# Performance work log

Measured on AMD Instinct MI355X. Metric: run time of the kernel, lower is better.

Reference implementation:

```python
import jax, jax.numpy as jnp
import numpy as np

B, H, W, C = 4, 128, 128, 768
NUM_BLOCKS = 8
BLOCK = C // NUM_BLOCKS  # 96
HSF = 1
SCALE = 0.02
LAMBD = 0.01
HARD_FRAC = 1.0


def setup_inputs() -> dict:
    key = jax.random.key(0)
    ks = jax.random.split(key, 5)
    return {
        "x": jax.random.normal(ks[0], (B, H, W, C), dtype=jnp.float32),
        "w1": SCALE * jax.random.normal(ks[1], (2, NUM_BLOCKS, BLOCK, BLOCK * HSF), dtype=jnp.float32),
        "b1": SCALE * jax.random.normal(ks[2], (2, NUM_BLOCKS, BLOCK * HSF), dtype=jnp.float32),
        "w2": SCALE * jax.random.normal(ks[3], (2, NUM_BLOCKS, BLOCK * HSF, BLOCK), dtype=jnp.float32),
        "b2": SCALE * jax.random.normal(ks[4], (2, NUM_BLOCKS, BLOCK), dtype=jnp.float32),
    }


def softshrink(v, lambd):
    return jnp.where(v > lambd, v - lambd, jnp.where(v < -lambd, v + lambd, 0.0))


def reference(x, w1, b1, w2, b2):
    bias = x
    dtype = x.dtype
    xf = jnp.fft.rfft2(x.astype(jnp.float32), axes=(1, 2), norm="ortho")  # [B,H,Wf,C] complex
    b, h, wf, c = xf.shape
    xf = xf.reshape(b, h, wf, NUM_BLOCKS, BLOCK)
    total_modes = H * W // 2 + 1
    kept = min(int(total_modes * HARD_FRAC), wf)  # static; with frac=1 kept == wf

    xr = jnp.real(xf[:, :, :kept])
    xi = jnp.imag(xf[:, :, :kept])

    o1r = jax.nn.relu(jnp.einsum("bhwni,nio->bhwno", xr, w1[0]) - jnp.einsum("bhwni,nio->bhwno", xi, w1[1]) + b1[0])
    o1i = jax.nn.relu(jnp.einsum("bhwni,nio->bhwno", xi, w1[0]) + jnp.einsum("bhwni,nio->bhwno", xr, w1[1]) + b1[1])

    o2r = jnp.einsum("bhwno,noi->bhwni", o1r, w2[0]) - jnp.einsum("bhwno,noi->bhwni", o1i, w2[1]) + b2[0]
    o2i = jnp.einsum("bhwno,noi->bhwni", o1i, w2[0]) + jnp.einsum("bhwno,noi->bhwni", o1r, w2[1]) + b2[1]

    o2r = softshrink(o2r, LAMBD)
    o2i = softshrink(o2i, LAMBD)

    if kept < wf:  # zero-fill the masked-out high frequencies
        pad = [(0, 0), (0, 0), (0, wf - kept), (0, 0), (0, 0)]
        o2r = jnp.pad(o2r, pad)
        o2i = jnp.pad(o2i, pad)

    xc = (o2r + 1j * o2i).reshape(b, h, wf, c)
    out = jnp.fft.irfft2(xc, s=(H, W), axes=(1, 2), norm="ortho").astype(dtype)
    return out + bias
```

## Files before the change

kernel.cpp:

```cpp
#include <hip/hip_runtime.h>

#define CH    768
#define BC    96
#define HHH   128
#define WWW   128
#define WF    65
#define LAMBD_ 0.01f
#define NPOS  33280
#define SOFF  204472320ull

typedef __bf16 bf16x8 __attribute__((ext_vector_type(8)));
typedef float  f32x4  __attribute__((ext_vector_type(4)));
typedef unsigned short ushort_t;

union U8 { ushort_t u[8]; bf16x8 v; uint4 q; };

__device__ __forceinline__ ushort_t rnbf(float f) {
  unsigned u = __builtin_bit_cast(unsigned, f);
  return (ushort_t)((u + 0x7FFFu + ((u >> 16) & 1u)) >> 16);
}

struct Tab {
  float c[64]; float s[64];
  static constexpr double tsin(double x) {
    double t = x, r = x; const double x2 = x * x;
    for (int i = 1; i <= 15; ++i) { t *= -x2 / ((2.0 * i) * (2.0 * i + 1.0)); r += t; }
    return r;
  }
  static constexpr double tcos(double x) {
    double t = 1.0, r = 1.0; const double x2 = x * x;
    for (int i = 1; i <= 15; ++i) { t *= -x2 / ((2.0 * i - 1.0) * (2.0 * i)); r += t; }
    return r;
  }
  constexpr Tab() : c{}, s{} {
    for (int k = 0; k < 64; ++k) {
      const double a = 6.283185307179586476925287 * (double)k / 128.0;
      c[k] = (float)tcos(a); s[k] = (float)tsin(a);
    }
  }
};
__device__ const Tab DTAB{};

__host__ __device__ constexpr int rev6(int n) {
  int r = 0;
  for (int b = 0; b < 6; ++b) r |= ((n >> b) & 1) << (5 - b);
  return r;
}

template<bool INV>
__device__ __forceinline__ void fft64_reg(float (&zr)[64], float (&zi)[64]) {
#pragma unroll
  for (int s = 1; s <= 6; ++s) {
    const int half = 1 << (s - 1);
#pragma unroll
    for (int i = 0; i < 64; i += (1 << s)) {
#pragma unroll
      for (int j = 0; j < half; ++j) {
        const int tw = j << (7 - s);
        const float wr = DTAB.c[tw];
        const float wi = INV ? DTAB.s[tw] : -DTAB.s[tw];
        const int i0 = i + j, i1 = i0 + half;
        const float xr = zr[i1], xi = zi[i1];
        const float vr = xr * wr - xi * wi;
        const float vi = xr * wi + xi * wr;
        const float ur = zr[i0], ui = zi[i0];
        zr[i0] = ur + vr; zi[i0] = ui + vi;
        zr[i1] = ur - vr; zi[i1] = ui - vi;
      }
    }
  }
}

__global__ __launch_bounds__(256, 1) void k_rfft_w(const float* __restrict__ x,
                                                   float2* __restrict__ S) {
  const int idx = blockIdx.x * 256 + threadIdx.x;
  const int c  = idx % CH;
  const int bh = idx / CH;
  const float* px = x + (size_t)bh * (WWW * CH) + c;
  float zr[64], zi[64];
#pragma unroll
  for (int n = 0; n < 64; ++n) {
    zr[rev6(n)] = px[(size_t)(2 * n) * CH];
    zi[rev6(n)] = px[(size_t)(2 * n + 1) * CH];
  }
  fft64_reg<false>(zr, zi);
  float2* pS = S + (size_t)bh * (WF * CH) + c;
  const float sc = 1.0f / 128.0f;
#pragma unroll
  for (int k = 0; k <= 32; ++k) {
    const int m = (64 - k) & 63;
    const float ar = zr[k], ai = zi[k];
    const float br = zr[m], bi = zi[m];
    const float Er = 0.5f * (ar + br), Ei = 0.5f * (ai - bi);
    const float Or = 0.5f * (ai + bi), Oi = 0.5f * (br - ar);
    const float wr = DTAB.c[k], wi = -DTAB.s[k];
    const float Tr = Or * wr - Oi * wi;
    const float Ti = Or * wi + Oi * wr;
    pS[(size_t)k * CH] = make_float2(sc * (Er + Tr), sc * (Ei + Ti));
    if (k != 32)
      pS[(size_t)(64 - k) * CH] = make_float2(sc * (Er - Tr), sc * (Ti - Ei));
  }
}

template<bool INV>
__global__ __launch_bounds__(256) void k_fft_h(float2* __restrict__ S) {
  __shared__ float lr[128 * 33];
  __shared__ float li[128 * 33];
  const int tid = threadIdx.x;
  const int c = tid & 31;
  const int g = tid >> 5;
  const int ct = blockIdx.x % 24;
  const int t2 = blockIdx.x / 24;
  const int wf = t2 % WF;
  const int b  = t2 / WF;
  float2* base = S + ((size_t)(b * HHH) * WF + wf) * CH + ct * 32 + c;
  const size_t hs = (size_t)WF * CH;
#pragma unroll
  for (int t = 0; t < 16; ++t) {
    const int h = t * 8 + g;
    const float2 v = base[(size_t)h * hs];
    const int hb = (int)(__brev((unsigned)h) >> 25);
    lr[hb * 33 + c] = v.x;
    li[hb * 33 + c] = v.y;
  }
  __syncthreads();
#pragma unroll
  for (int s = 1; s <= 7; ++s) {
    const int half = 1 << (s - 1);
#pragma unroll
    for (int t = 0; t < 8; ++t) {
      const int bf = g * 8 + t;
      const int j  = bf & (half - 1);
      const int i0 = ((bf >> (s - 1)) << s) + j;
      const int i1 = i0 + half;
      const int tw = j << (7 - s);
      const float wr = DTAB.c[tw];
      const float wi = INV ? DTAB.s[tw] : -DTAB.s[tw];
      const float ur = lr[i0 * 33 + c], ui = li[i0 * 33 + c];
      const float xr = lr[i1 * 33 + c], xi = li[i1 * 33 + c];
      const float vr = xr * wr - xi * wi;
      const float vi = xr * wi + xi * wr;
      lr[i0 * 33 + c] = ur + vr;  li[i0 * 33 + c] = ui + vi;
      lr[i1 * 33 + c] = ur - vr;  li[i1 * 33 + c] = ui - vi;
    }
    __syncthreads();
  }
#pragma unroll
  for (int t = 0; t < 16; ++t) {
    const int h = t * 8 + g;
    base[(size_t)h * hs] = make_float2(lr[h * 33 + c], li[h * 33 + c]);
  }
}

__global__ __launch_bounds__(256) void k_pack(const float* __restrict__ w1,
                                              const float* __restrict__ w2,
                                              ushort_t* __restrict__ Bpk) {
  const int t = blockIdx.x * 256 + threadIdx.x;
  const int nl   = t / 36864;
  const int rem  = t % 36864;
  const int ki   = rem / 6144;
  const int rem2 = rem % 6144;
  const int ni   = rem2 / 512;
  const int rem3 = rem2 % 512;
  const int lane = rem3 >> 3, j = rem3 & 7;
  const int n = nl >> 1, layer = nl & 1;
  const int k   = ki * 32 + (lane >> 4) * 8 + j;
  const int col = ni * 16 + (lane & 15);
  const int kk = (k < 96) ? k : k - 96;
  const int cc = (col < 96) ? col : col - 96;
  const int f  = ((k < 96) != (col < 96)) ? 1 : 0;
  const float sgn = (k >= 96 && col < 96) ? -1.f : 1.f;
  const float* w = layer ? w2 : w1;
  const float val = sgn * w[((size_t)(f * 8 + n) * 96 + kk) * 96 + cc];
  Bpk[t] = rnbf(val);
}

__global__ __launch_bounds__(256) void k_mlp2(float2* __restrict__ S,
                                              const ushort_t* __restrict__ Bpk,
                                              const float* __restrict__ b1,
                                              const float* __restrict__ b2) {
  __shared__ ushort_t o1[64 * 200];
  const int tid = threadIdx.x;
  const int l = tid & 63, wid = tid >> 6;
  const int lr = l & 15, lg = l >> 4;
  const int n  = blockIdx.x & 7;
  const int p0 = (blockIdx.x >> 3) * 64 + wid * 16;

  U8 aR[3], aI[3];
  const float4* xbase = (const float4*)(S + (size_t)(p0 + lr) * CH + n * BC);
#pragma unroll
  for (int kp = 0; kp < 3; ++kp) {
    const float4* q = xbase + (kp * 32 + lg * 8) / 2;
    const float4 f0 = q[0], f1 = q[1], f2 = q[2], f3 = q[3];
    aR[kp].u[0] = rnbf(f0.x); aR[kp].u[1] = rnbf(f0.z);
    aR[kp].u[2] = rnbf(f1.x); aR[kp].u[3] = rnbf(f1.z);
    aR[kp].u[4] = rnbf(f2.x); aR[kp].u[5] = rnbf(f2.z);
    aR[kp].u[6] = rnbf(f3.x); aR[kp].u[7] = rnbf(f3.z);
    aI[kp].u[0] = rnbf(f0.y); aI[kp].u[1] = rnbf(f0.w);
    aI[kp].u[2] = rnbf(f1.y); aI[kp].u[3] = rnbf(f1.w);
    aI[kp].u[4] = rnbf(f2.y); aI[kp].u[5] = rnbf(f2.w);
    aI[kp].u[6] = rnbf(f3.y); aI[kp].u[7] = rnbf(f3.w);
  }

  f32x4 acc[12];
#pragma unroll
  for (int ni = 0; ni < 12; ++ni) {
    const int col = ni * 16 + lr;
    const float bv = (col < 96) ? b1[n * 96 + col] : b1[768 + n * 96 + col - 96];
    acc[ni] = (f32x4){bv, bv, bv, bv};
  }
  const uint4* bq1 = (const uint4*)(Bpk + (size_t)(n * 2 + 0) * 36864) + l;
#pragma unroll
  for (int ni = 0; ni < 12; ++ni)
#pragma unroll
    for (int ki = 0; ki < 6; ++ki) {
      U8 b; b.q = bq1[(ki * 12 + ni) * 64];
      const bf16x8 a = (ki < 3) ? aR[ki].v : aI[ki - 3].v;
      acc[ni] = __builtin_amdgcn_mfma_f32_16x16x32_bf16(a, b.v, acc[ni], 0, 0, 0);
    }
#pragma unroll
  for (int ni = 0; ni < 12; ++ni) {
    const int col = ni * 16 + lr;
#pragma unroll
    for (int r = 0; r < 4; ++r) {
      const int grow = wid * 16 + lg * 4 + r;
      o1[grow * 200 + col] = rnbf(fmaxf(acc[ni][r], 0.f));
    }
  }
  __syncthreads();

  U8 a2[6];
#pragma unroll
  for (int ki = 0; ki < 6; ++ki)
    a2[ki].q = *(const uint4*)&o1[(wid * 16 + lr) * 200 + ki * 32 + lg * 8];
#pragma unroll
  for (int ni = 0; ni < 12; ++ni) {
    const int col = ni * 16 + lr;
    const float bv = (col < 96) ? b2[n * 96 + col] : b2[768 + n * 96 + col - 96];
    acc[ni] = (f32x4){bv, bv, bv, bv};
  }
  const uint4* bq2 = (const uint4*)(Bpk + (size_t)(n * 2 + 1) * 36864) + l;
#pragma unroll
  for (int ni = 0; ni < 12; ++ni)
#pragma unroll
    for (int ki = 0; ki < 6; ++ki) {
      U8 b; b.q = bq2[(ki * 12 + ni) * 64];
      acc[ni] = __builtin_amdgcn_mfma_f32_16x16x32_bf16(a2[ki].v, b.v, acc[ni], 0, 0, 0);
    }
  float* Sf = (float*)S;
#pragma unroll
  for (int ni = 0; ni < 12; ++ni) {
    const int col = ni * 16 + lr;
    const int c    = (col < 96) ? col : col - 96;
    const int comp = (col < 96) ? 0 : 1;
#pragma unroll
    for (int r = 0; r < 4; ++r) {
      const int p = p0 + lg * 4 + r;
      float v = acc[ni][r];
      v = v > LAMBD_ ? v - LAMBD_ : (v < -LAMBD_ ? v + LAMBD_ : 0.f);
      Sf[2 * ((size_t)p * CH + n * BC + c) + comp] = v;
    }
  }
}

__global__ __launch_bounds__(256, 1) void k_irfft_w(const float2* __restrict__ S,
                                                    const float* __restrict__ x,
                                                    float* __restrict__ out) {
  const int idx = blockIdx.x * 256 + threadIdx.x;
  const int c  = idx % CH;
  const int bh = idx / CH;
  const float2* pS = S + (size_t)bh * (WF * CH) + c;
  float zr[64], zi[64];
#pragma unroll
  for (int k = 0; k <= 32; ++k) {
    float2 Yk = pS[(size_t)k * CH];
    float2 Ym = pS[(size_t)(64 - k) * CH];
    if (k == 0) { Yk.y = 0.f; Ym.y = 0.f; }
    const float er = Yk.x + Ym.x, ei = Yk.y - Ym.y;
    const float dr = Yk.x - Ym.x, di = Yk.y + Ym.y;
    const float wr = DTAB.c[k], wi = DTAB.s[k];
    const float o_r = dr * wr - di * wi;
    const float o_i = dr * wi + di * wr;
    zr[rev6(k)] = er - o_i;  zi[rev6(k)] = ei + o_r;
    if (k > 0 && k < 32) {
      zr[rev6(64 - k)] = er + o_i;  zi[rev6(64 - k)] = o_r - ei;
    }
  }
  fft64_reg<true>(zr, zi);
  const float sc = 1.0f / 128.0f;
  const float* px = x + (size_t)bh * (WWW * CH) + c;
  float* po = out + (size_t)bh * (WWW * CH) + c;
#pragma unroll
  for (int n = 0; n < 64; ++n) {
    po[(size_t)(2 * n) * CH]     = fmaf(zr[n], sc, px[(size_t)(2 * n) * CH]);
    po[(size_t)(2 * n + 1) * CH] = fmaf(zi[n], sc, px[(size_t)(2 * n + 1) * CH]);
  }
}

extern "C" void kernel_launch(void* const* d_in, const int* in_sizes, int n_in,
                              void* d_out, int out_size, void* d_ws, size_t ws_size,
                              hipStream_t stream) {
  (void)in_sizes; (void)n_in; (void)out_size; (void)ws_size;
  const float* x  = (const float*)d_in[0];
  const float* w1 = (const float*)d_in[1];
  const float* b1 = (const float*)d_in[2];
  const float* w2 = (const float*)d_in[3];
  const float* b2 = (const float*)d_in[4];
  float* out = (float*)d_out;
  float2* S  = (float2*)d_ws;
  ushort_t* Bpk = (ushort_t*)((char*)d_ws + SOFF);

  k_pack<<<dim3(2304), dim3(256), 0, stream>>>(w1, w2, Bpk);
  k_rfft_w<<<dim3(1536), dim3(256), 0, stream>>>(x, S);
  k_fft_h<false><<<dim3(6240), dim3(256), 0, stream>>>(S);
  k_mlp2<<<dim3((NPOS / 64) * 8), dim3(256), 0, stream>>>(S, Bpk, b1, b2);
  k_fft_h<true><<<dim3(6240), dim3(256), 0, stream>>>(S);
  k_irfft_w<<<dim3(1536), dim3(256), 0, stream>>>(S, x, out);
}
```

Before: 777.8 us.

## Fuse H-axis forward FFT, spectral MLP and inverse H-FFT into one kernel

Replaces the separate forward column FFT, block MLP, and inverse column FFT kernels with one kernel. Each workgroup loads a full 128-row column of one 96-channel block into shared memory, does the forward FFT there, runs both MFMA layers on the 128 rows, writes the softshrunk result back bit-reversed, runs the inverse FFT, and stores once. This removes two full read/write round trips of the spectrum through global memory and two launches. The cost is about 100KB of LDS per workgroup at one workgroup per CU, only 2080 workgroups, and each wave now holds two row tiles of accumulators, which raises register pressure.

```diff
diff --git a/kernel.cpp b/kernel.cpp
--- a/kernel.cpp
+++ b/kernel.cpp
@@ -2,12 +2,12 @@
 
 #define CH    768
 #define BC    96
-#define HHH   128
 #define WWW   128
 #define WF    65
 #define LAMBD_ 0.01f
 #define NPOS  33280
 #define SOFF  204472320ull
+#define LDST  100
 
 typedef __bf16 bf16x8 __attribute__((ext_vector_type(8)));
 typedef float  f32x4  __attribute__((ext_vector_type(4)));
@@ -99,56 +99,6 @@
     pS[(size_t)k * CH] = make_float2(sc * (Er + Tr), sc * (Ei + Ti));
     if (k != 32)
       pS[(size_t)(64 - k) * CH] = make_float2(sc * (Er - Tr), sc * (Ti - Ei));
-  }
-}
-
-template<bool INV>
-__global__ __launch_bounds__(256) void k_fft_h(float2* __restrict__ S) {
-  __shared__ float lr[128 * 33];
-  __shared__ float li[128 * 33];
-  const int tid = threadIdx.x;
-  const int c = tid & 31;
-  const int g = tid >> 5;
-  const int ct = blockIdx.x % 24;
-  const int t2 = blockIdx.x / 24;
-  const int wf = t2 % WF;
-  const int b  = t2 / WF;
-  float2* base = S + ((size_t)(b * HHH) * WF + wf) * CH + ct * 32 + c;
-  const size_t hs = (size_t)WF * CH;
-#pragma unroll
-  for (int t = 0; t < 16; ++t) {
-    const int h = t * 8 + g;
-    const float2 v = base[(size_t)h * hs];
-    const int hb = (int)(__brev((unsigned)h) >> 25);
-    lr[hb * 33 + c] = v.x;
-    li[hb * 33 + c] = v.y;
-  }
-  __syncthreads();
-#pragma unroll
-  for (int s = 1; s <= 7; ++s) {
-    const int half = 1 << (s - 1);
-#pragma unroll
-    for (int t = 0; t < 8; ++t) {
-      const int bf = g * 8 + t;
-      const int j  = bf & (half - 1);
-      const int i0 = ((bf >> (s - 1)) << s) + j;
-      const int i1 = i0 + half;
-      const int tw = j << (7 - s);
-      const float wr = DTAB.c[tw];
-      const float wi = INV ? DTAB.s[tw] : -DTAB.s[tw];
-      const float ur = lr[i0 * 33 + c], ui = li[i0 * 33 + c];
-      const float xr = lr[i1 * 33 + c], xi = li[i1 * 33 + c];
-      const float vr = xr * wr - xi * wi;
-      const float vi = xr * wi + xi * wr;
-      lr[i0 * 33 + c] = ur + vr;  li[i0 * 33 + c] = ui + vi;
-      lr[i1 * 33 + c] = ur - vr;  li[i1 * 33 + c] = ui - vi;
-    }
-    __syncthreads();
-  }
-#pragma unroll
-  for (int t = 0; t < 16; ++t) {
-    const int h = t * 8 + g;
-    base[(size_t)h * hs] = make_float2(lr[h * 33 + c], li[h * 33 + c]);
   }
 }
 
@@ -175,91 +125,169 @@
   Bpk[t] = rnbf(val);
 }
 
-__global__ __launch_bounds__(256) void k_mlp2(float2* __restrict__ S,
-                                              const ushort_t* __restrict__ Bpk,
-                                              const float* __restrict__ b1,
-                                              const float* __restrict__ b2) {
-  __shared__ ushort_t o1[64 * 200];
+__global__ __launch_bounds__(256, 1) void k_fused(float2* __restrict__ S,
+                                                  const ushort_t* __restrict__ Bpk,
+                                                  const float* __restrict__ b1,
+                                                  const float* __restrict__ b2) {
+  __shared__ __attribute__((aligned(16))) float lsr[128 * LDST];
+  __shared__ __attribute__((aligned(16))) float lsi[128 * LDST];
   const int tid = threadIdx.x;
+  const int wg = blockIdx.x;
+  const int n = wg & 7;
+  const int rest = wg >> 3;
+  const int wf = rest % WF;
+  const int b  = rest / WF;
+  float2* gbase = S + ((size_t)(b * 128) * WF + wf) * CH + n * BC;
+  const size_t hs = (size_t)WF * CH;
+
+#pragma unroll
+  for (int i = 0; i < 24; ++i) {
+    const int q = tid + i * 256;
+    const int h = q / 48;
+    const int cp = q - h * 48;
+    const float4 v = *(const float4*)(gbase + (size_t)h * hs + 2 * cp);
+    const int hb = (int)(__brev((unsigned)h) >> 25);
+    *(float2*)&lsr[hb * LDST + 2 * cp] = make_float2(v.x, v.z);
+    *(float2*)&lsi[hb * LDST + 2 * cp] = make_float2(v.y, v.w);
+  }
+
+  const int ct = tid & 31, bt = tid >> 5;
+  auto fftpass = [&](bool inv) {
+    for (int s = 1; s <= 7; ++s) {
+      __syncthreads();
+      const int half = 1 << (s - 1);
+#pragma unroll
+      for (int cth = 0; cth < 3; ++cth) {
+#pragma unroll
+        for (int j = 0; j < 8; ++j) {
+          const int bf = bt * 8 + j;
+          const int jj = bf & (half - 1);
+          const int i0 = ((bf >> (s - 1)) << s) + jj;
+          const int i1 = i0 + half;
+          const int tw = jj << (7 - s);
+          const float wr = DTAB.c[tw];
+          const float wi = inv ? DTAB.s[tw] : -DTAB.s[tw];
+          const int c = cth * 32 + ct;
+          const int a0 = i0 * LDST + c, a1a = i1 * LDST + c;
+          const float xr = lsr[a1a], xi = lsi[a1a];
+          const float vr = xr * wr - xi * wi;
+          const float vi = xr * wi + xi * wr;
+          const float ur = lsr[a0], ui = lsi[a0];
+          lsr[a0] = ur + vr;  lsi[a0] = ui + vi;
+          lsr[a1a] = ur - vr; lsi[a1a] = ui - vi;
+        }
+      }
+    }
+    __syncthreads();
+  };
+
+  fftpass(false);
+
   const int l = tid & 63, wid = tid >> 6;
-  const int lr = l & 15, lg = l >> 4;
-  const int n  = blockIdx.x & 7;
-  const int p0 = (blockIdx.x >> 3) * 64 + wid * 16;
-
-  U8 aR[3], aI[3];
-  const float4* xbase = (const float4*)(S + (size_t)(p0 + lr) * CH + n * BC);
-#pragma unroll
-  for (int kp = 0; kp < 3; ++kp) {
-    const float4* q = xbase + (kp * 32 + lg * 8) / 2;
-    const float4 f0 = q[0], f1 = q[1], f2 = q[2], f3 = q[3];
-    aR[kp].u[0] = rnbf(f0.x); aR[kp].u[1] = rnbf(f0.z);
-    aR[kp].u[2] = rnbf(f1.x); aR[kp].u[3] = rnbf(f1.z);
-    aR[kp].u[4] = rnbf(f2.x); aR[kp].u[5] = rnbf(f2.z);
-    aR[kp].u[6] = rnbf(f3.x); aR[kp].u[7] = rnbf(f3.z);
-    aI[kp].u[0] = rnbf(f0.y); aI[kp].u[1] = rnbf(f0.w);
-    aI[kp].u[2] = rnbf(f1.y); aI[kp].u[3] = rnbf(f1.w);
-    aI[kp].u[4] = rnbf(f2.y); aI[kp].u[5] = rnbf(f2.w);
-    aI[kp].u[6] = rnbf(f3.y); aI[kp].u[7] = rnbf(f3.w);
-  }
-
-  f32x4 acc[12];
+  const int lr_ = l & 15, lg = l >> 4;
+
+  U8 a1[2][6];
+#pragma unroll
+  for (int rt = 0; rt < 2; ++rt) {
+    const int row = wid * 32 + rt * 16 + lr_;
+#pragma unroll
+    for (int ki = 0; ki < 6; ++ki) {
+      const float* src = (ki < 3) ? &lsr[row * LDST + ki * 32 + lg * 8]
+                                  : &lsi[row * LDST + (ki - 3) * 32 + lg * 8];
+      const float4 f0 = *(const float4*)src;
+      const float4 f1 = *(const float4*)(src + 4);
+      a1[rt][ki].u[0] = rnbf(f0.x); a1[rt][ki].u[1] = rnbf(f0.y);
+      a1[rt][ki].u[2] = rnbf(f0.z); a1[rt][ki].u[3] = rnbf(f0.w);
+      a1[rt][ki].u[4] = rnbf(f1.x); a1[rt][ki].u[5] = rnbf(f1.y);
+      a1[rt][ki].u[6] = rnbf(f1.z); a1[rt][ki].u[7] = rnbf(f1.w);
+    }
+  }
+
+  f32x4 acc[2][12];
 #pragma unroll
   for (int ni = 0; ni < 12; ++ni) {
-    const int col = ni * 16 + lr;
+    const int col = ni * 16 + lr_;
     const float bv = (col < 96) ? b1[n * 96 + col] : b1[768 + n * 96 + col - 96];
-    acc[ni] = (f32x4){bv, bv, bv, bv};
+    acc[0][ni] = (f32x4){bv, bv, bv, bv};
+    acc[1][ni] = acc[0][ni];
   }
   const uint4* bq1 = (const uint4*)(Bpk + (size_t)(n * 2 + 0) * 36864) + l;
 #pragma unroll
   for (int ni = 0; ni < 12; ++ni)
 #pragma unroll
     for (int ki = 0; ki < 6; ++ki) {
-      U8 b; b.q = bq1[(ki * 12 + ni) * 64];
-      const bf16x8 a = (ki < 3) ? aR[ki].v : aI[ki - 3].v;
-      acc[ni] = __builtin_amdgcn_mfma_f32_16x16x32_bf16(a, b.v, acc[ni], 0, 0, 0);
-    }
+      U8 bb; bb.q = bq1[(ki * 12 + ni) * 64];
+      acc[0][ni] = __builtin_amdgcn_mfma_f32_16x16x32_bf16(a1[0][ki].v, bb.v, acc[0][ni], 0, 0, 0);
+      acc[1][ni] = __builtin_amdgcn_mfma_f32_16x16x32_bf16(a1[1][ki].v, bb.v, acc[1][ni], 0, 0, 0);
+    }
+
+  ushort_t* o1 = (ushort_t*)lsr;
+#pragma unroll
+  for (int rt = 0; rt < 2; ++rt)
+#pragma unroll
+    for (int ni = 0; ni < 12; ++ni) {
+      const int col = ni * 16 + lr_;
+#pragma unroll
+      for (int r = 0; r < 4; ++r) {
+        const int row = wid * 32 + rt * 16 + lg * 4 + r;
+        o1[row * 200 + col] = rnbf(fmaxf(acc[rt][ni][r], 0.f));
+      }
+    }
+
+  U8 a2[2][6];
+#pragma unroll
+  for (int rt = 0; rt < 2; ++rt) {
+    const int row = wid * 32 + rt * 16 + lr_;
+#pragma unroll
+    for (int ki = 0; ki < 6; ++ki)
+      a2[rt][ki].q = *(const uint4*)&o1[row * 200 + ki * 32 + lg * 8];
+  }
+  __syncthreads();
+
 #pragma unroll
   for (int ni = 0; ni < 12; ++ni) {
-    const int col = ni * 16 + lr;
-#pragma unroll
-    for (int r = 0; r < 4; ++r) {
-      const int grow = wid * 16 + lg * 4 + r;
-      o1[grow * 200 + col] = rnbf(fmaxf(acc[ni][r], 0.f));
-    }
-  }
-  __syncthreads();
-
-  U8 a2[6];
-#pragma unroll
-  for (int ki = 0; ki < 6; ++ki)
-    a2[ki].q = *(const uint4*)&o1[(wid * 16 + lr) * 200 + ki * 32 + lg * 8];
-#pragma unroll
-  for (int ni = 0; ni < 12; ++ni) {
-    const int col = ni * 16 + lr;
+    const int col = ni * 16 + lr_;
     const float bv = (col < 96) ? b2[n * 96 + col] : b2[768 + n * 96 + col - 96];
-    acc[ni] = (f32x4){bv, bv, bv, bv};
+    acc[0][ni] = (f32x4){bv, bv, bv, bv};
+    acc[1][ni] = acc[0][ni];
   }
   const uint4* bq2 = (const uint4*)(Bpk + (size_t)(n * 2 + 1) * 36864) + l;
 #pragma unroll
   for (int ni = 0; ni < 12; ++ni)
 #pragma unroll
     for (int ki = 0; ki < 6; ++ki) {
-      U8 b; b.q = bq2[(ki * 12 + ni) * 64];
-      acc[ni] = __builtin_amdgcn_mfma_f32_16x16x32_bf16(a2[ki].v, b.v, acc[ni], 0, 0, 0);
-    }
-  float* Sf = (float*)S;
-#pragma unroll
-  for (int ni = 0; ni < 12; ++ni) {
-    const int col = ni * 16 + lr;
-    const int c    = (col < 96) ? col : col - 96;
-    const int comp = (col < 96) ? 0 : 1;
-#pragma unroll
-    for (int r = 0; r < 4; ++r) {
-      const int p = p0 + lg * 4 + r;
-      float v = acc[ni][r];
-      v = v > LAMBD_ ? v - LAMBD_ : (v < -LAMBD_ ? v + LAMBD_ : 0.f);
-      Sf[2 * ((size_t)p * CH + n * BC + c) + comp] = v;
-    }
+      U8 bb; bb.q = bq2[(ki * 12 + ni) * 64];
+      acc[0][ni] = __builtin_amdgcn_mfma_f32_16x16x32_bf16(a2[0][ki].v, bb.v, acc[0][ni], 0, 0, 0);
+      acc[1][ni] = __builtin_amdgcn_mfma_f32_16x16x32_bf16(a2[1][ki].v, bb.v, acc[1][ni], 0, 0, 0);
+    }
+
+#pragma unroll
+  for (int rt = 0; rt < 2; ++rt)
+#pragma unroll
+    for (int ni = 0; ni < 12; ++ni) {
+      const int col = ni * 16 + lr_;
+      const int c    = (col < 96) ? col : col - 96;
+      float* plane = (col < 96) ? lsr : lsi;
+#pragma unroll
+      for (int r = 0; r < 4; ++r) {
+        const int p = wid * 32 + rt * 16 + lg * 4 + r;
+        const int tr = (int)(__brev((unsigned)p) >> 25);
+        float v = acc[rt][ni][r];
+        v = v > LAMBD_ ? v - LAMBD_ : (v < -LAMBD_ ? v + LAMBD_ : 0.f);
+        plane[tr * LDST + c] = v;
+      }
+    }
+
+  fftpass(true);
+
+#pragma unroll
+  for (int i = 0; i < 24; ++i) {
+    const int q = tid + i * 256;
+    const int h = q / 48;
+    const int cp = q - h * 48;
+    const float2 r2 = *(const float2*)&lsr[h * LDST + 2 * cp];
+    const float2 i2 = *(const float2*)&lsi[h * LDST + 2 * cp];
+    *(float4*)(gbase + (size_t)h * hs + 2 * cp) = make_float4(r2.x, i2.x, r2.y, i2.y);
   }
 }
 
@@ -312,8 +340,6 @@
 
   k_pack<<<dim3(2304), dim3(256), 0, stream>>>(w1, w2, Bpk);
   k_rfft_w<<<dim3(1536), dim3(256), 0, stream>>>(x, S);
-  k_fft_h<false><<<dim3(6240), dim3(256), 0, stream>>>(S);
-  k_mlp2<<<dim3((NPOS / 64) * 8), dim3(256), 0, stream>>>(S, Bpk, b1, b2);
-  k_fft_h<true><<<dim3(6240), dim3(256), 0, stream>>>(S);
+  k_fused<<<dim3(4 * WF * 8), dim3(256), 0, stream>>>(S, Bpk, b1, b2);
   k_irfft_w<<<dim3(1536), dim3(256), 0, stream>>>(S, x, out);
 }
```

After: 947.7 us. 1.22x slower.
